# Kernel optimization log

Hardware: AMD Instinct MI355X
Metric: run time of the kernel (lower is better)

The kernel has to match this reference:

```python
import jax, jax.numpy as jnp
import numpy as np

EPS = 0.01


def setup_inputs() -> dict:
    key = jax.random.key(0)
    ks = jax.random.split(key, 7)
    B, N, H = 4, 1024, 64
    pos = jax.random.normal(ks[0], (B, N, 3), dtype=jnp.float32)
    # MLP params (Linear stores weight as [out,in]; we keep [in,out] for x @ W)
    W1 = jax.random.normal(ks[1], (1, H), dtype=jnp.float32) * (1.0 / np.sqrt(1))
    b1 = jax.random.normal(ks[2], (H,), dtype=jnp.float32) * 0.01
    W2 = jax.random.normal(ks[3], (H, H), dtype=jnp.float32) * (1.0 / np.sqrt(H))
    b2 = jax.random.normal(ks[4], (H,), dtype=jnp.float32) * 0.01
    W3 = jax.random.normal(ks[5], (H, 1), dtype=jnp.float32) * (1.0 / np.sqrt(H))
    b3 = jax.random.normal(ks[6], (1,), dtype=jnp.float32) * 0.01
    return {"pos": pos, "W1": W1, "b1": b1, "W2": W2, "b2": b2, "W3": W3, "b3": b3}


def reference(pos, W1, b1, W2, b2, W3, b3):
    B, N, _ = pos.shape
    # pairwise soft distances, only upper-triangular pairs (i < j)
    idx_i, idx_j = jnp.triu_indices(N, k=1)                      # [P], P = N(N-1)/2
    diff = pos[:, idx_i, :] - pos[:, idx_j, :]                   # [B, P, 3]
    dist_soft = jnp.sqrt(jnp.sum(diff * diff, axis=-1) + EPS * EPS)  # [B, P]
    d = dist_soft[..., None]                                     # [B, P, 1]
    h = jax.nn.silu(d @ W1 + b1)                                 # [B, P, H]
    h = jax.nn.silu(h @ W2 + b2)                                 # [B, P, H]
    u = (h @ W3 + b3)[..., 0]                                    # [B, P]
    U = jnp.sum(u, axis=1, keepdims=True) / N                    # [B, 1]
    return U
```

## Files before the change

### kernel.cpp

```cpp
#include <hip/hip_runtime.h>


constexpr int N_ATOMS = 1024;
constexpr int H = 64;
constexpr int NB = 4;
constexpr int PAIRS = N_ATOMS * (N_ATOMS - 1) / 2;
constexpr float EPS = 0.01f;

constexpr int NT = 2048;
constexpr int NNODES = NT + 1;
constexpr float TMAX = 16.0f;
constexpr float INV_H = (float)NT / TMAX;
constexpr double DH = (double)TMAX / (double)NT;

constexpr int BLOCK = 256;
constexpr int BLOCKS_PER_BATCH = 256;
constexpr int CHUNK = BLOCKS_PER_BATCH * BLOCK;
constexpr int NITER = (PAIRS + CHUNK - 1) / CHUNK;

__global__ __launch_bounds__(64) void build_table(
    const float* __restrict__ W1, const float* __restrict__ b1,
    const float* __restrict__ W2, const float* __restrict__ b2,
    const float* __restrict__ W3, const float* __restrict__ b3,
    float2* __restrict__ tab, double* __restrict__ sums)
{
    const int node = blockIdx.x;
    const int lane = threadIdx.x;
    if (node == 0 && lane < NB) sums[lane] = 0.0;

    const double d = (double)node * DH;

    double a1 = d * (double)W1[lane] + (double)b1[lane];
    double s1 = 1.0 / (1.0 + exp(-a1));
    double h1 = a1 * s1;
    double g1 = (s1 + a1 * s1 * (1.0 - s1)) * (double)W1[lane];

    double acc = (double)b2[lane], dacc = 0.0;
    for (int k = 0; k < H; ++k) {
        double hk = __shfl(h1, k);
        double gk = __shfl(g1, k);
        double w  = (double)W2[k * H + lane];
        acc  += hk * w;
        dacc += gk * w;
    }
    double s2  = 1.0 / (1.0 + exp(-acc));
    double h2  = acc * s2;
    double dh2 = (s2 + acc * s2 * (1.0 - s2)) * dacc;

    double pu = h2  * (double)W3[lane];
    double du = dh2 * (double)W3[lane];
    for (int off = 32; off; off >>= 1) {
        pu += __shfl_down(pu, off);
        du += __shfl_down(du, off);
    }
    if (lane == 0)
        tab[node] = make_float2((float)((double)b3[0] + pu), (float)(du * DH));
}

__global__ __launch_bounds__(BLOCK) void hnn_lut(
    const float* __restrict__ pos, const float2* __restrict__ tab,
    double* __restrict__ sums)
{
    __shared__ float2 lt[NNODES];
    for (int idx = threadIdx.x; idx < NNODES; idx += BLOCK) lt[idx] = tab[idx];
    __syncthreads();

    const int b   = blockIdx.x >> 8;
    const int blk = blockIdx.x & 255;
    const float* pb = pos + b * N_ATOMS * 3;

    float acc = 0.0f;
#pragma unroll
    for (int it = 0; it < NITER; ++it) {
        const int p = blk * BLOCK + (int)threadIdx.x + it * CHUNK;
        if (p < PAIRS) {
            float fp = (float)p;
            int i = (int)((2047.0f - sqrtf(4190209.0f - 8.0f * fp)) * 0.5f);
            i = max(0, min(i, N_ATOMS - 2));
            while ((i * (2 * N_ATOMS - 1 - i)) / 2 > p) --i;
            while (((i + 1) * (2 * N_ATOMS - 1 - (i + 1))) / 2 <= p) ++i;
            const int j = p - (i * (2 * N_ATOMS - 1 - i)) / 2 + i + 1;

            float dx = pb[i * 3 + 0] - pb[j * 3 + 0];
            float dy = pb[i * 3 + 1] - pb[j * 3 + 1];
            float dz = pb[i * 3 + 2] - pb[j * 3 + 2];
            float d  = sqrtf(fmaf(dx, dx, fmaf(dy, dy, fmaf(dz, dz, EPS * EPS))));

            float t  = d * INV_H;
            int   k  = min((int)t, NT - 1);
            float fr = t - (float)k;
            float2 n0 = lt[k], n1 = lt[k + 1];
            float dp = n1.x - n0.x;
            float c2 = fmaf(3.0f, dp, -fmaf(2.0f, n0.y, n1.y));
            float c3 = fmaf(-2.0f, dp, n0.y + n1.y);
            acc += n0.x + fr * fmaf(fr, fmaf(fr, c3, c2), n0.y);
        }
    }

    for (int off = 32; off; off >>= 1) acc += __shfl_down(acc, off);
    __shared__ float wpart[BLOCK / 64];
    if ((threadIdx.x & 63) == 0) wpart[threadIdx.x >> 6] = acc;
    __syncthreads();
    if (threadIdx.x == 0)
        atomicAdd(sums + b, (double)(wpart[0] + wpart[1] + wpart[2] + wpart[3]));
}

__global__ void hnn_finalize(const double* __restrict__ sums, float* __restrict__ out) {
    if (threadIdx.x < NB)
        out[threadIdx.x] = (float)(sums[threadIdx.x] * (1.0 / (double)N_ATOMS));
}

extern "C" void kernel_launch(void* const* d_in, const int* in_sizes, int n_in,
                              void* d_out, int out_size, void* d_ws, size_t ws_size,
                              hipStream_t stream) {
    const float* pos = (const float*)d_in[0];
    const float* W1  = (const float*)d_in[1];
    const float* b1  = (const float*)d_in[2];
    const float* W2  = (const float*)d_in[3];
    const float* b2  = (const float*)d_in[4];
    const float* W3  = (const float*)d_in[5];
    const float* b3  = (const float*)d_in[6];

    float2* tab  = (float2*)d_ws;
    double* sums = (double*)((char*)d_ws + (size_t)NNODES * sizeof(float2));
    float*  out  = (float*)d_out;

    hipLaunchKernelGGL(build_table, dim3(NNODES), dim3(64), 0, stream,
                       W1, b1, W2, b2, W3, b3, tab, sums);
    hipLaunchKernelGGL(hnn_lut, dim3(NB * BLOCKS_PER_BATCH), dim3(BLOCK), 0, stream,
                       pos, tab, sums);
    hipLaunchKernelGGL(hnn_finalize, dim3(1), dim3(64), 0, stream, sums, out);
}
```

Before: 93.60 us.

## Compute full symmetric pair matrix with tiled shared positions and halve table

Replaces the triangular pair-index decoding (sqrt plus correction loops per pair) with a dense i×j tile sweep over all N² pairs. The sum is halved and the self-pair diagonal contribution is subtracted in finalize. Positions and precomputed cubic Hermite coefficients are staged in shared memory. The table is shrunk to 1024 nodes, per-block partials replace double atomics, and finalize does a deterministic reduction. This doubles the pair evaluations, and the coarser table and diagonal cancellation may reduce accuracy.

```diff
diff --git a/kernel.cpp b/kernel.cpp
--- a/kernel.cpp
+++ b/kernel.cpp
@@ -4,30 +4,38 @@
 constexpr int N_ATOMS = 1024;
 constexpr int H = 64;
 constexpr int NB = 4;
-constexpr int PAIRS = N_ATOMS * (N_ATOMS - 1) / 2;
 constexpr float EPS = 0.01f;
 
-constexpr int NT = 2048;
+constexpr int NT = 1024;
 constexpr int NNODES = NT + 1;
 constexpr float TMAX = 16.0f;
 constexpr float INV_H = (float)NT / TMAX;
 constexpr double DH = (double)TMAX / (double)NT;
 
 constexpr int BLOCK = 256;
-constexpr int BLOCKS_PER_BATCH = 256;
-constexpr int CHUNK = BLOCKS_PER_BATCH * BLOCK;
-constexpr int NITER = (PAIRS + CHUNK - 1) / CHUNK;
+constexpr int ITILES = N_ATOMS / 64;
+constexpr int JCHUNKS = 8;
+constexpr int NBLK = NB * ITILES * JCHUNKS;
+constexpr int JPW = 32;
+
+__device__ __forceinline__ float4 make_coef(float2 n0, float2 n1) {
+    float dp = n1.x - n0.x;
+    float c2 = fmaf(3.0f, dp, -fmaf(2.0f, n0.y, n1.y));
+    float c3 = fmaf(-2.0f, dp, n0.y + n1.y);
+    return make_float4(n0.x, n0.y, c2, c3);
+}
+__device__ __forceinline__ float heval(float4 c, float fr) {
+    return fmaf(fr, fmaf(fr, fmaf(fr, c.w, c.z), c.y), c.x);
+}
 
 __global__ __launch_bounds__(64) void build_table(
     const float* __restrict__ W1, const float* __restrict__ b1,
     const float* __restrict__ W2, const float* __restrict__ b2,
     const float* __restrict__ W3, const float* __restrict__ b3,
-    float2* __restrict__ tab, double* __restrict__ sums)
+    float2* __restrict__ nodes)
 {
     const int node = blockIdx.x;
     const int lane = threadIdx.x;
-    if (node == 0 && lane < NB) sums[lane] = 0.0;
-
     const double d = (double)node * DH;
 
     double a1 = d * (double)W1[lane] + (double)b1[lane];
@@ -54,60 +62,82 @@
         du += __shfl_down(du, off);
     }
     if (lane == 0)
-        tab[node] = make_float2((float)((double)b3[0] + pu), (float)(du * DH));
+        nodes[node] = make_float2((float)((double)b3[0] + pu), (float)(du * DH));
 }
 
-__global__ __launch_bounds__(BLOCK) void hnn_lut(
-    const float* __restrict__ pos, const float2* __restrict__ tab,
-    double* __restrict__ sums)
+__global__ __launch_bounds__(BLOCK) void hnn_pair(
+    const float* __restrict__ pos, const float2* __restrict__ nodes,
+    double* __restrict__ partials)
 {
-    __shared__ float2 lt[NNODES];
-    for (int idx = threadIdx.x; idx < NNODES; idx += BLOCK) lt[idx] = tab[idx];
+    __shared__ float4 posl4[N_ATOMS * 3 / 4];
+    __shared__ float4 coef[NT];
+    __shared__ float wred[BLOCK / 64];
+
+    const int bid  = blockIdx.x;
+    const int b    = bid >> 7;
+    const int r    = bid & 127;
+    const int ibase = (r >> 3) * 64;
+    const int jbase = (r & 7) * 128;
+    const int tid  = (int)threadIdx.x;
+
+    const float4* p4 = (const float4*)(pos + (size_t)b * N_ATOMS * 3);
+#pragma unroll
+    for (int rr = 0; rr < 3; ++rr)
+        posl4[tid + BLOCK * rr] = p4[tid + BLOCK * rr];
+#pragma unroll
+    for (int rr = 0; rr < NT / BLOCK; ++rr) {
+        int k = tid + BLOCK * rr;
+        coef[k] = make_coef(nodes[k], nodes[k + 1]);
+    }
     __syncthreads();
 
-    const int b   = blockIdx.x >> 8;
-    const int blk = blockIdx.x & 255;
-    const float* pb = pos + b * N_ATOMS * 3;
+    const float* posf = (const float*)posl4;
+    const int lane = tid & 63;
+    const int w    = tid >> 6;
+    const int i    = ibase + lane;
+    const float xi = posf[3 * i], yi = posf[3 * i + 1], zi = posf[3 * i + 2];
 
     float acc = 0.0f;
+    const int j0 = jbase + w * JPW;
 #pragma unroll
-    for (int it = 0; it < NITER; ++it) {
-        const int p = blk * BLOCK + (int)threadIdx.x + it * CHUNK;
-        if (p < PAIRS) {
-            float fp = (float)p;
-            int i = (int)((2047.0f - sqrtf(4190209.0f - 8.0f * fp)) * 0.5f);
-            i = max(0, min(i, N_ATOMS - 2));
-            while ((i * (2 * N_ATOMS - 1 - i)) / 2 > p) --i;
-            while (((i + 1) * (2 * N_ATOMS - 1 - (i + 1))) / 2 <= p) ++i;
-            const int j = p - (i * (2 * N_ATOMS - 1 - i)) / 2 + i + 1;
-
-            float dx = pb[i * 3 + 0] - pb[j * 3 + 0];
-            float dy = pb[i * 3 + 1] - pb[j * 3 + 1];
-            float dz = pb[i * 3 + 2] - pb[j * 3 + 2];
-            float d  = sqrtf(fmaf(dx, dx, fmaf(dy, dy, fmaf(dz, dz, EPS * EPS))));
-
-            float t  = d * INV_H;
-            int   k  = min((int)t, NT - 1);
-            float fr = t - (float)k;
-            float2 n0 = lt[k], n1 = lt[k + 1];
-            float dp = n1.x - n0.x;
-            float c2 = fmaf(3.0f, dp, -fmaf(2.0f, n0.y, n1.y));
-            float c3 = fmaf(-2.0f, dp, n0.y + n1.y);
-            acc += n0.x + fr * fmaf(fr, fmaf(fr, c3, c2), n0.y);
-        }
+    for (int s = 0; s < JPW; ++s) {
+        const int j = j0 + s;
+        float dx = xi - posf[3 * j];
+        float dy = yi - posf[3 * j + 1];
+        float dz = zi - posf[3 * j + 2];
+        float d  = sqrtf(fmaf(dx, dx, fmaf(dy, dy, fmaf(dz, dz, EPS * EPS))));
+        float t  = d * INV_H;
+        int   k  = min((int)t, NT - 1);
+        float fr = t - (float)k;
+        acc += heval(coef[k], fr);
     }
 
     for (int off = 32; off; off >>= 1) acc += __shfl_down(acc, off);
-    __shared__ float wpart[BLOCK / 64];
-    if ((threadIdx.x & 63) == 0) wpart[threadIdx.x >> 6] = acc;
+    if (lane == 0) wred[w] = acc;
     __syncthreads();
-    if (threadIdx.x == 0)
-        atomicAdd(sums + b, (double)(wpart[0] + wpart[1] + wpart[2] + wpart[3]));
+    if (tid == 0)
+        partials[bid] = (double)((wred[0] + wred[1]) + (wred[2] + wred[3]));
 }
 
-__global__ void hnn_finalize(const double* __restrict__ sums, float* __restrict__ out) {
-    if (threadIdx.x < NB)
-        out[threadIdx.x] = (float)(sums[threadIdx.x] * (1.0 / (double)N_ATOMS));
+__global__ __launch_bounds__(BLOCK) void hnn_finalize(
+    const float2* __restrict__ nodes, const double* __restrict__ partials,
+    float* __restrict__ out)
+{
+    const int tid  = (int)threadIdx.x;
+    const int b    = tid >> 6;
+    const int lane = tid & 63;
+    double s = partials[b * 128 + lane] + partials[b * 128 + 64 + lane];
+    for (int off = 32; off; off >>= 1) s += __shfl_down(s, off);
+    if (lane == 0) {
+        float d  = sqrtf(fmaf(0.0f, 0.0f, fmaf(0.0f, 0.0f,
+                         fmaf(0.0f, 0.0f, EPS * EPS))));
+        float t  = d * INV_H;
+        int   k  = min((int)t, NT - 1);
+        float fr = t - (float)k;
+        float fe = heval(make_coef(nodes[k], nodes[k + 1]), fr);
+        out[b] = (float)((s - (double)N_ATOMS * (double)fe)
+                         * (0.5 / (double)N_ATOMS));
+    }
 }
 
 extern "C" void kernel_launch(void* const* d_in, const int* in_sizes, int n_in,
@@ -121,13 +151,14 @@
     const float* W3  = (const float*)d_in[5];
     const float* b3  = (const float*)d_in[6];
 
-    float2* tab  = (float2*)d_ws;
-    double* sums = (double*)((char*)d_ws + (size_t)NNODES * sizeof(float2));
-    float*  out  = (float*)d_out;
+    float2* nodes    = (float2*)d_ws;
+    double* partials = (double*)((char*)d_ws + 16384);
+    float*  out      = (float*)d_out;
 
     hipLaunchKernelGGL(build_table, dim3(NNODES), dim3(64), 0, stream,
-                       W1, b1, W2, b2, W3, b3, tab, sums);
-    hipLaunchKernelGGL(hnn_lut, dim3(NB * BLOCKS_PER_BATCH), dim3(BLOCK), 0, stream,
-                       pos, tab, sums);
-    hipLaunchKernelGGL(hnn_finalize, dim3(1), dim3(64), 0, stream, sums, out);
+                       W1, b1, W2, b2, W3, b3, nodes);
+    hipLaunchKernelGGL(hnn_pair, dim3(NBLK), dim3(BLOCK), 0, stream,
+                       pos, nodes, partials);
+    hipLaunchKernelGGL(hnn_finalize, dim3(1), dim3(BLOCK), 0, stream,
+                       nodes, partials, out);
 }
```

Measured after the change: 79.01 us. 15.6% less time.
